# Kernel tuning notes

Measured on AMD Instinct MI355X. Metric: run time of the kernel, lower is better.

Reference implementation:

```python
import jax, jax.numpy as jnp
import numpy as np

B, N, A, M, H, KD, VD, O = 256, 2048, 256, 256, 8, 32, 32, 256
EPS = 1e-10

def setup_inputs() -> dict:
    key = jax.random.key(0)
    ks = jax.random.split(key, 8)
    return {
        "q_data": jax.random.normal(ks[0], (B, N, A), dtype=jnp.float32),
        "m_data": jax.random.normal(ks[1], (B, N, M), dtype=jnp.float32),
        "q_mask": jnp.ones((B, N, 1), dtype=jnp.float32),
        "bias": jnp.zeros((B, 1, N), dtype=jnp.float32),
        "query_w": 0.02 * jax.random.normal(ks[2], (A, H, KD), dtype=jnp.float32),
        "key_w": 0.02 * jax.random.normal(ks[3], (M, KD), dtype=jnp.float32),
        "value_w": 0.02 * jax.random.normal(ks[4], (M, VD), dtype=jnp.float32),
        "gating_w": 0.02 * jax.random.normal(ks[5], (A, H, VD), dtype=jnp.float32),
        "gating_b": jnp.zeros((H, VD), dtype=jnp.float32),
        "output_w": 0.02 * jax.random.normal(ks[6], (H, VD, O), dtype=jnp.float32),
        "output_b": jnp.zeros((O,), dtype=jnp.float32),
    }

def reference(q_data, m_data, q_mask, bias, query_w, key_w, value_w,
              gating_w, gating_b, output_w, output_b):
    # masked mean over the query axis: q_mask [B,N,1] broadcasts over channels
    q_avg = jnp.sum(q_mask * q_data, axis=1) / (jnp.sum(q_mask, axis=1) + EPS)  # [B,A]
    kd = query_w.shape[-1]
    q = jnp.einsum('ba,ahc->bhc', q_avg, query_w) * kd ** (-0.5)  # [B,H,KD]
    k = jnp.einsum('bka,ac->bkc', m_data, key_w)                  # [B,N,KD]
    v = jnp.einsum('bka,ac->bkc', m_data, value_w)                # [B,N,VD]
    # the incoming `bias` arg is overwritten by the module, as in the original
    attn_bias = 1e9 * (q_mask[:, None, :, 0] - 1.0)               # [B,1,N]
    logits = jnp.einsum('bhc,bkc->bhk', q, k) + attn_bias         # [B,H,N]
    weights = jax.nn.softmax(logits, axis=-1)
    weighted_avg = jnp.einsum('bhk,bkc->bhc', weights, v)         # [B,H,VD]
    # gating == True
    gate = jax.nn.sigmoid(jnp.einsum('bqc,chv->bqhv', q_data, gating_w) + gating_b)
    gated = weighted_avg[:, None] * gate                          # [B,N,H,VD]
    out = jnp.einsum('bqhc,hco->bqo', gated, output_w) + output_b # [B,N,O]
    return out
```

## Files before the change

kernel.cpp:

```cpp
#include <hip/hip_runtime.h>

#define B_ 256
#define N_ 2048
#define A_ 256
#define M_ 256
#define H_ 8
#define KD_ 32
#define VD_ 32
#define O_ 256

typedef float f32x4 __attribute__((ext_vector_type(4)));
typedef __bf16 bf16x8 __attribute__((ext_vector_type(8)));
typedef unsigned short u16x8 __attribute__((ext_vector_type(8)));

union FragU { u16x8 u; bf16x8 b; };

__device__ __forceinline__ unsigned short f2bf(float f) {
  union { __bf16 b; unsigned short u; } c;
  c.b = (__bf16)f;
  return c.u;
}
__device__ __forceinline__ float bf2f(unsigned short h) {
  return __uint_as_float(((unsigned int)h) << 16);
}

__device__ __forceinline__ void gll16(const void* gsrc, void* ldst) {
  __builtin_amdgcn_global_load_lds(
      (const __attribute__((address_space(1))) void*)gsrc,
      (__attribute__((address_space(3))) void*)ldst, 16, 0, 0);
}

__global__ void pack_weights(const float* __restrict__ gating_w,
                             const float* __restrict__ output_w,
                             const float* __restrict__ key_w,
                             const float* __restrict__ value_w,
                             unsigned short* __restrict__ wg,
                             unsigned short* __restrict__ wo,
                             unsigned short* __restrict__ wkv) {
  int idx = blockIdx.x * 256 + threadIdx.x;
  int j = idx & 7;
  int lane = (idx >> 3) & 63;
  int rest = idx >> 9;
  int kc = rest & 7, ct = rest >> 3;
  int row = kc * 32 + ((lane >> 4) << 3) + j;
  int col = ct * 16 + (lane & 15);
  wg[idx] = f2bf(gating_w[row * 256 + col]);
  wo[idx] = f2bf(output_w[row * 256 + col]);
  if (idx < 16384) {
    float v = (col < 32) ? key_w[row * 32 + col] : value_w[row * 32 + (col - 32)];
    wkv[idx] = f2bf(v);
  }
}

__global__ void reduce_q(const float* __restrict__ qd, const float* __restrict__ qm,
                         const float* __restrict__ qw, float* __restrict__ q_out) {
  int b = blockIdx.x;
  int t = threadIdx.x;
  int l = t & 63, g = t >> 6;
  const float* qdb = qd + (size_t)b * N_ * A_;
  const float* qmb = qm + (size_t)b * N_;
  f32x4 sum = {0.f, 0.f, 0.f, 0.f};
  float msum = 0.f;
  for (int n = g; n < N_; n += 16) {
    float m = qmb[n];
    msum += m;
    f32x4 v = *(const f32x4*)(qdb + (size_t)n * A_ + l * 4);
    sum += m * v;
  }
  __shared__ float s[16][256];
  __shared__ float ms[16];
  __shared__ float qavg[256];
  *(f32x4*)&s[g][l * 4] = sum;
  if (l == 0) ms[g] = msum;
  __syncthreads();
  if (t < 256) {
    float tot = 0.f;
#pragma unroll
    for (int k = 0; k < 16; k++) tot += s[k][t];
    float mt = 0.f;
#pragma unroll
    for (int k = 0; k < 16; k++) mt += ms[k];
    qavg[t] = tot / (mt + 1e-10f);
  }
  __syncthreads();
  if (t < 256) {
    float acc = 0.f;
    for (int a2 = 0; a2 < 256; a2++) acc += qavg[a2] * qw[a2 * 256 + t];
    q_out[b * 256 + t] = acc * 0.17677669529663687f;
  }
}

__global__ void kv_gemm(const float* __restrict__ md,
                        const unsigned short* __restrict__ wkv,
                        unsigned short* __restrict__ kv) {
  int t = threadIdx.x;
  int w = t >> 6, l = t & 63, q = l >> 4, l15 = l & 15;
  size_t r0 = (size_t)blockIdx.x * 128;
  f32x4 acc[2][4] = {};
  for (int kc = 0; kc < 8; kc++) {
    FragU bfr[4];
#pragma unroll
    for (int ct = 0; ct < 4; ct++)
      bfr[ct].u = *(const u16x8*)(wkv + (((ct * 8 + kc) * 64 + l) << 3));
    FragU af[2];
#pragma unroll
    for (int rt = 0; rt < 2; rt++) {
      size_t row = r0 + (size_t)(w * 32 + rt * 16 + l15);
      const float4* s4 = (const float4*)(md + row * 256 + kc * 32 + q * 8);
      float4 u0 = s4[0], u1 = s4[1];
      af[rt].u = (u16x8){f2bf(u0.x), f2bf(u0.y), f2bf(u0.z), f2bf(u0.w),
                         f2bf(u1.x), f2bf(u1.y), f2bf(u1.z), f2bf(u1.w)};
    }
#pragma unroll
    for (int ct = 0; ct < 4; ct++) {
      acc[0][ct] = __builtin_amdgcn_mfma_f32_16x16x32_bf16(af[0].b, bfr[ct].b, acc[0][ct], 0, 0, 0);
      acc[1][ct] = __builtin_amdgcn_mfma_f32_16x16x32_bf16(af[1].b, bfr[ct].b, acc[1][ct], 0, 0, 0);
    }
  }
#pragma unroll
  for (int rt = 0; rt < 2; rt++)
#pragma unroll
    for (int ct = 0; ct < 4; ct++)
#pragma unroll
      for (int r = 0; r < 4; r++) {
        size_t row = r0 + (size_t)(w * 32 + rt * 16 + q * 4 + r);
        kv[row * 64 + ct * 16 + l15] = f2bf(acc[rt][ct][r]);
      }
}

__global__ void attn_softmax(const unsigned short* __restrict__ kv,
                             const float* __restrict__ qv,
                             const float* __restrict__ qm,
                             float* __restrict__ wa) {
  int b = blockIdx.x, t = threadIdx.x;
  __shared__ float lg[8][2048];
  __shared__ float red[4][256];
  __shared__ float inv_s[8];
  const float* qb = qv + b * 256;
  const float* qmb = qm + (size_t)b * N_;
  for (int n = t; n < N_; n += 1024) {
    const u16x8* kr = (const u16x8*)(kv + ((size_t)(b * N_ + n)) * 64);
    float kf[32];
#pragma unroll
    for (int c8 = 0; c8 < 4; c8++) {
      u16x8 kk = kr[c8];
#pragma unroll
      for (int j = 0; j < 8; j++) kf[c8 * 8 + j] = bf2f(kk[j]);
    }
    float bias_n = 1e9f * (qmb[n] - 1.0f);
#pragma unroll
    for (int h = 0; h < 8; h++) {
      float d = 0.f;
#pragma unroll
      for (int c = 0; c < 32; c++) d += qb[h * 32 + c] * kf[c];
      lg[h][n] = d + bias_n;
    }
  }
  __syncthreads();
  if (t < 256) {
    int h = t >> 5, i = t & 31;
    float m = -3.0e38f;
    for (int n = i; n < N_; n += 32) m = fmaxf(m, lg[h][n]);
#pragma unroll
    for (int off = 16; off; off >>= 1) m = fmaxf(m, __shfl_xor(m, off));
    float s = 0.f;
    for (int n = i; n < N_; n += 32) {
      float e = __expf(lg[h][n] - m);
      lg[h][n] = e;
      s += e;
    }
#pragma unroll
    for (int off = 16; off; off >>= 1) s += __shfl_xor(s, off);
    if (i == 0) inv_s[h] = 1.0f / s;
  }
  __syncthreads();
  {
    int c = t & 31, h = (t >> 5) & 7, nq = t >> 8;
    const unsigned short* vb = kv + ((size_t)b * N_ + nq * 512) * 64 + 32 + c;
    const float* lgh = &lg[h][nq * 512];
    float acc = 0.f;
#pragma unroll 8
    for (int n = 0; n < 512; n++) acc += lgh[n] * bf2f(vb[(size_t)n * 64]);
    red[nq][t & 255] = acc;
  }
  __syncthreads();
  if (t < 256) {
    float r = red[0][t] + red[1][t] + red[2][t] + red[3][t];
    wa[b * 256 + t] = r * inv_s[t >> 5];
  }
}

__launch_bounds__(256, 4)
__global__ void gate_out(const float* __restrict__ qd,
                         const unsigned short* __restrict__ wg,
                         const unsigned short* __restrict__ wo,
                         const float* __restrict__ wa,
                         const float* __restrict__ gb,
                         const float* __restrict__ ob,
                         float* __restrict__ out) {
  int blk = blockIdx.x;
  int b = blk >> 5, tile = blk & 31;
  int t = threadIdx.x;
  int w = t >> 6, l = t & 63, q = l >> 4, l15 = l & 15;
  __shared__ __attribute__((aligned(16))) unsigned short wsg[8192];
  __shared__ __attribute__((aligned(16))) unsigned short wso[8192];
  __shared__ __attribute__((aligned(16))) unsigned short Pt[4][16][40];
  __shared__ float wa_s[256], gb_s[256], ob_s[256];
  wa_s[t] = wa[b * 256 + t];
  gb_s[t] = gb[t];
  ob_s[t] = ob[t];
  size_t rowbase = (size_t)b * N_ + tile * 64;

  {
    const char* wgb = (const char*)wg;
    const char* wob = (const char*)wo;
#pragma unroll
    for (int i = 0; i < 4; i++) {
      int ch = i * 4 + w;
      gll16(wgb + ch * 1024 + l * 16, (char*)wsg + ch * 1024);
      gll16(wob + ch * 8192 + l * 16, (char*)wso + ch * 1024);
    }
  }

  FragU af[8];
  {
    const float* src = qd + (rowbase + (size_t)(w * 16 + l15)) * 256 + q * 8;
#pragma unroll
    for (int kc = 0; kc < 8; kc++) {
      float4 u0 = *(const float4*)(src + kc * 32);
      float4 u1 = *(const float4*)(src + kc * 32 + 4);
      af[kc].u = (u16x8){f2bf(u0.x), f2bf(u0.y), f2bf(u0.z), f2bf(u0.w),
                         f2bf(u1.x), f2bf(u1.y), f2bf(u1.z), f2bf(u1.w)};
    }
  }
  f32x4 acc[16] = {};
  __syncthreads();

  for (int g = 0; g < 8; g++) {
    f32x4 gacc[2] = {};
#pragma unroll
    for (int kc = 0; kc < 8; kc++) {
      FragU b0, b1;
      b0.u = *(const u16x8*)(wsg + (kc * 64 + l) * 8);
      b1.u = *(const u16x8*)(wsg + ((8 + kc) * 64 + l) * 8);
      gacc[0] = __builtin_amdgcn_mfma_f32_16x16x32_bf16(af[kc].b, b0.b, gacc[0], 0, 0, 0);
      gacc[1] = __builtin_amdgcn_mfma_f32_16x16x32_bf16(af[kc].b, b1.b, gacc[1], 0, 0, 0);
    }
#pragma unroll
    for (int ctl = 0; ctl < 2; ctl++) {
      int colg = ctl * 16 + l15;
      int col = g * 32 + colg;
      float wav = wa_s[col], gbv = gb_s[col];
#pragma unroll
      for (int r = 0; r < 4; r++) {
        float x = gacc[ctl][r] + gbv;
        float gate = 1.0f / (1.0f + __expf(-x));
        Pt[w][q * 4 + r][colg] = f2bf(wav * gate);
      }
    }
    FragU pf;
    pf.u = *(const u16x8*)&Pt[w][l15][q * 8];

    __syncthreads();
    if (g < 7) {
      const char* wgb = (const char*)wg + (size_t)(g + 1) * 16384;
#pragma unroll
      for (int i = 0; i < 4; i++) {
        int ch = i * 4 + w;
        gll16(wgb + ch * 1024 + l * 16, (char*)wsg + ch * 1024);
      }
    }
#pragma unroll
    for (int ct = 0; ct < 16; ct++) {
      FragU bo;
      bo.u = *(const u16x8*)(wso + (ct * 64 + l) * 8);
      acc[ct] = __builtin_amdgcn_mfma_f32_16x16x32_bf16(pf.b, bo.b, acc[ct], 0, 0, 0);
    }
    __syncthreads();
    if (g < 7) {
      const char* wob = (const char*)wo + (size_t)(g + 1) * 1024;
#pragma unroll
      for (int i = 0; i < 4; i++) {
        int ch = i * 4 + w;
        gll16(wob + ch * 8192 + l * 16, (char*)wso + ch * 1024);
      }
    }
  }
#pragma unroll
  for (int ct = 0; ct < 16; ct++) {
    int col = ct * 16 + l15;
    float obv = ob_s[col];
    size_t orow = (rowbase + (size_t)(w * 16 + q * 4)) * 256 + col;
#pragma unroll
    for (int r = 0; r < 4; r++)
      out[orow + (size_t)r * 256] = acc[ct][r] + obv;
  }
}

extern "C" void kernel_launch(void* const* d_in, const int* in_sizes, int n_in,
                              void* d_out, int out_size, void* d_ws, size_t ws_size,
                              hipStream_t stream) {
  const float* q_data   = (const float*)d_in[0];
  const float* m_data   = (const float*)d_in[1];
  const float* q_mask   = (const float*)d_in[2];
  const float* query_w  = (const float*)d_in[4];
  const float* key_w    = (const float*)d_in[5];
  const float* value_w  = (const float*)d_in[6];
  const float* gating_w = (const float*)d_in[7];
  const float* gating_b = (const float*)d_in[8];
  const float* output_w = (const float*)d_in[9];
  const float* output_b = (const float*)d_in[10];
  float* out = (float*)d_out;

  char* ws = (char*)d_ws;
  float* q_ws            = (float*)(ws);
  float* wa_ws           = (float*)(ws + (256 << 10));
  unsigned short* wg_ws  = (unsigned short*)(ws + (512 << 10));
  unsigned short* wo_ws  = (unsigned short*)(ws + (640 << 10));
  unsigned short* wkv_ws = (unsigned short*)(ws + (768 << 10));
  unsigned short* kv_ws  = (unsigned short*)(ws + (800 << 10));

  pack_weights<<<256, 256, 0, stream>>>(gating_w, output_w, key_w, value_w,
                                        wg_ws, wo_ws, wkv_ws);
  reduce_q<<<B_, 1024, 0, stream>>>(q_data, q_mask, query_w, q_ws);
  kv_gemm<<<(B_ * N_) / 128, 256, 0, stream>>>(m_data, wkv_ws, kv_ws);
  attn_softmax<<<B_, 1024, 0, stream>>>(kv_ws, q_ws, q_mask, wa_ws);
  gate_out<<<(B_ * N_) / 64, 256, 0, stream>>>(q_data, wg_ws, wo_ws, wa_ws,
                                               gating_b, output_b, out);
}
```

Before: 1.439 ms.

## Merge weight packing, query reduction and KV GEMM into one heterogeneous launch

Three front-end kernels become one grid whose block index picks the role: 256 blocks reduce q_data and project the query, 256 blocks pack the gating and output weights, and 4096 blocks run the KV GEMM. Each KV GEMM block packs key/value weights into LDS itself instead of reading a pre-packed global buffer. This removes two launches and serialisation between them, so the memory-bound q reduction can overlap the m_data GEMM. In exchange the reduction blocks drop from 1024 to 256 threads, and every GEMM block repeats the weight conversion and uses 32KB of LDS, which may lower occupancy.

```diff
diff --git a/kernel.cpp b/kernel.cpp
--- a/kernel.cpp
+++ b/kernel.cpp
@@ -30,78 +30,86 @@
       (__attribute__((address_space(3))) void*)ldst, 16, 0, 0);
 }
 
-__global__ void pack_weights(const float* __restrict__ gating_w,
-                             const float* __restrict__ output_w,
-                             const float* __restrict__ key_w,
-                             const float* __restrict__ value_w,
-                             unsigned short* __restrict__ wg,
-                             unsigned short* __restrict__ wo,
-                             unsigned short* __restrict__ wkv) {
-  int idx = blockIdx.x * 256 + threadIdx.x;
-  int j = idx & 7;
-  int lane = (idx >> 3) & 63;
-  int rest = idx >> 9;
-  int kc = rest & 7, ct = rest >> 3;
-  int row = kc * 32 + ((lane >> 4) << 3) + j;
-  int col = ct * 16 + (lane & 15);
-  wg[idx] = f2bf(gating_w[row * 256 + col]);
-  wo[idx] = f2bf(output_w[row * 256 + col]);
-  if (idx < 16384) {
-    float v = (col < 32) ? key_w[row * 32 + col] : value_w[row * 32 + (col - 32)];
-    wkv[idx] = f2bf(v);
-  }
-}
-
-__global__ void reduce_q(const float* __restrict__ qd, const float* __restrict__ qm,
-                         const float* __restrict__ qw, float* __restrict__ q_out) {
-  int b = blockIdx.x;
+__global__ void front(const float* __restrict__ qd, const float* __restrict__ qm,
+                      const float* __restrict__ qw, float* __restrict__ q_out,
+                      const float* __restrict__ gating_w,
+                      const float* __restrict__ output_w,
+                      const float* __restrict__ key_w,
+                      const float* __restrict__ value_w,
+                      unsigned short* __restrict__ wg,
+                      unsigned short* __restrict__ wo,
+                      const float* __restrict__ md,
+                      unsigned short* __restrict__ kv) {
+  __shared__ __attribute__((aligned(16))) unsigned short smem_u16[16384];
+  int blk = blockIdx.x;
   int t = threadIdx.x;
-  int l = t & 63, g = t >> 6;
-  const float* qdb = qd + (size_t)b * N_ * A_;
-  const float* qmb = qm + (size_t)b * N_;
-  f32x4 sum = {0.f, 0.f, 0.f, 0.f};
-  float msum = 0.f;
-  for (int n = g; n < N_; n += 16) {
-    float m = qmb[n];
-    msum += m;
-    f32x4 v = *(const f32x4*)(qdb + (size_t)n * A_ + l * 4);
-    sum += m * v;
-  }
-  __shared__ float s[16][256];
-  __shared__ float ms[16];
-  __shared__ float qavg[256];
-  *(f32x4*)&s[g][l * 4] = sum;
-  if (l == 0) ms[g] = msum;
-  __syncthreads();
-  if (t < 256) {
-    float tot = 0.f;
-#pragma unroll
-    for (int k = 0; k < 16; k++) tot += s[k][t];
-    float mt = 0.f;
-#pragma unroll
-    for (int k = 0; k < 16; k++) mt += ms[k];
-    qavg[t] = tot / (mt + 1e-10f);
-  }
-  __syncthreads();
-  if (t < 256) {
-    float acc = 0.f;
-    for (int a2 = 0; a2 < 256; a2++) acc += qavg[a2] * qw[a2 * 256 + t];
-    q_out[b * 256 + t] = acc * 0.17677669529663687f;
-  }
-}
-
-__global__ void kv_gemm(const float* __restrict__ md,
-                        const unsigned short* __restrict__ wkv,
-                        unsigned short* __restrict__ kv) {
-  int t = threadIdx.x;
+
+  if (blk < 256) {
+    int b = blk;
+    int l = t & 63, g = t >> 6;
+    const float* qdb = qd + (size_t)b * N_ * A_;
+    const float* qmb = qm + (size_t)b * N_;
+    f32x4 sum = {0.f, 0.f, 0.f, 0.f};
+    float msum = 0.f;
+    for (int n = g; n < N_; n += 4) {
+      float m = qmb[n];
+      msum += m;
+      f32x4 v = *(const f32x4*)(qdb + (size_t)n * A_ + l * 4);
+      sum += m * v;
+    }
+    float* sb = (float*)smem_u16;
+    float* ms = sb + 1024;
+    float* qavg = sb + 1040;
+    *(f32x4*)&sb[g * 256 + l * 4] = sum;
+    if (l == 0) ms[g] = msum;
+    __syncthreads();
+    {
+      float tot = sb[t] + sb[256 + t] + sb[512 + t] + sb[768 + t];
+      float mt = ms[0] + ms[1] + ms[2] + ms[3];
+      qavg[t] = tot / (mt + 1e-10f);
+    }
+    __syncthreads();
+    {
+      float acc = 0.f;
+      for (int a2 = 0; a2 < 256; a2++) acc += qavg[a2] * qw[a2 * 256 + t];
+      q_out[b * 256 + t] = acc * 0.17677669529663687f;
+    }
+    return;
+  }
+  if (blk < 512) {
+    int idx = (blk - 256) * 256 + t;
+    int j = idx & 7;
+    int lane = (idx >> 3) & 63;
+    int rest = idx >> 9;
+    int kc = rest & 7, ct = rest >> 3;
+    int row = kc * 32 + ((lane >> 4) << 3) + j;
+    int col = ct * 16 + (lane & 15);
+    wg[idx] = f2bf(gating_w[row * 256 + col]);
+    wo[idx] = f2bf(output_w[row * 256 + col]);
+    return;
+  }
+  {
+#pragma unroll 8
+    for (int k = 0; k < 64; k++) {
+      int e = k * 256 + t;
+      int row = e >> 6, col = e & 63;
+      float v = (col < 32) ? key_w[row * 32 + col] : value_w[row * 32 + (col - 32)];
+      int kc = row >> 5, rowin = row & 31;
+      int hi = rowin >> 3, j = rowin & 7;
+      int ct = col >> 4, l15c = col & 15;
+      int fidx = (((ct * 8 + kc) * 64) + hi * 16 + l15c) * 8 + j;
+      smem_u16[fidx] = f2bf(v);
+    }
+  }
+  __syncthreads();
   int w = t >> 6, l = t & 63, q = l >> 4, l15 = l & 15;
-  size_t r0 = (size_t)blockIdx.x * 128;
+  size_t r0 = (size_t)(blk - 512) * 128;
   f32x4 acc[2][4] = {};
   for (int kc = 0; kc < 8; kc++) {
     FragU bfr[4];
 #pragma unroll
     for (int ct = 0; ct < 4; ct++)
-      bfr[ct].u = *(const u16x8*)(wkv + (((ct * 8 + kc) * 64 + l) << 3));
+      bfr[ct].u = *(const u16x8*)(smem_u16 + (((ct * 8 + kc) * 64 + l) << 3));
     FragU af[2];
 #pragma unroll
     for (int rt = 0; rt < 2; rt++) {
@@ -317,13 +325,11 @@
   float* wa_ws           = (float*)(ws + (256 << 10));
   unsigned short* wg_ws  = (unsigned short*)(ws + (512 << 10));
   unsigned short* wo_ws  = (unsigned short*)(ws + (640 << 10));
-  unsigned short* wkv_ws = (unsigned short*)(ws + (768 << 10));
   unsigned short* kv_ws  = (unsigned short*)(ws + (800 << 10));
 
-  pack_weights<<<256, 256, 0, stream>>>(gating_w, output_w, key_w, value_w,
-                                        wg_ws, wo_ws, wkv_ws);
-  reduce_q<<<B_, 1024, 0, stream>>>(q_data, q_mask, query_w, q_ws);
-  kv_gemm<<<(B_ * N_) / 128, 256, 0, stream>>>(m_data, wkv_ws, kv_ws);
+  front<<<4608, 256, 0, stream>>>(q_data, q_mask, query_w, q_ws,
+                                  gating_w, output_w, key_w, value_w,
+                                  wg_ws, wo_ws, m_data, kv_ws);
   attn_softmax<<<B_, 1024, 0, stream>>>(kv_ws, q_ws, q_mask, wa_ws);
   gate_out<<<(B_ * N_) / 64, 256, 0, stream>>>(q_data, wg_ws, wo_ws, wa_ws,
                                                gating_b, output_b, out);
```

Result: slower. 1.534 ms (+6.6%).
